# Performance work log

Measured on AMD Instinct MI355X. Metric: run time of the kernel, lower is better.

The kernel has to match this reference:

```python
import jax, jax.numpy as jnp
import numpy as np

HIDDEN = 32
N_STEPS = 64  # fixed-step RK4 replaces adaptive Dopri5 (same MLP-eval structure)
STD = 0.1     # init_params: Linear weights ~ N(0, 0.1), biases = 0


def _mlp(w1, b1, w2, b2, w3, b3, y):
    # NODE.forward: fc1 -> relu -> fc2 -> relu -> fc3 (t is unused in the source)
    h = jax.nn.relu(y @ w1 + b1)
    h = jax.nn.relu(h @ w2 + b2)
    return h @ w3 + b3


def setup_inputs() -> dict:
    key = jax.random.key(0)
    ks = jax.random.split(key, 8)
    B, D = 131072, 3
    x = jax.random.normal(ks[0], (B, D), dtype=jnp.float32)
    # eval times in (0.1, 1.0], sorted like a posterior-sample schedule
    samples = jnp.sort(
        jax.random.uniform(ks[1], (8, 1), jnp.float32, 0.1, 1.0), axis=0)
    w1 = (STD * jax.random.normal(ks[2], (D, HIDDEN))).astype(jnp.float32)
    b1 = jnp.zeros((HIDDEN,), jnp.float32)
    w2 = (STD * jax.random.normal(ks[3], (HIDDEN, HIDDEN))).astype(jnp.float32)
    b2 = jnp.zeros((HIDDEN,), jnp.float32)
    w3 = (STD * jax.random.normal(ks[4], (HIDDEN, D))).astype(jnp.float32)
    b3 = jnp.zeros((D,), jnp.float32)
    w_out = (STD * jax.random.normal(ks[5], (D, 1))).astype(jnp.float32)
    b_out = jnp.zeros((1,), jnp.float32)
    return {"x": x, "samples": samples, "w1": w1, "b1": b1, "w2": w2,
            "b2": b2, "w3": w3, "b3": b3, "w_out": w_out, "b_out": b_out}


def reference(x, samples, w1, b1, w2, b2, w3, b3, w_out, b_out):
    t_eval = samples[:, 0]                     # (S,)
    max_T = jnp.max(t_eval)
    dt = max_T / N_STEPS

    def step(y, _):
        k1 = _mlp(w1, b1, w2, b2, w3, b3, y)
        k2 = _mlp(w1, b1, w2, b2, w3, b3, y + 0.5 * dt * k1)
        k3 = _mlp(w1, b1, w2, b2, w3, b3, y + 0.5 * dt * k2)
        k4 = _mlp(w1, b1, w2, b2, w3, b3, y + dt * k3)
        y_new = y + (dt / 6.0) * (k1 + 2.0 * k2 + 2.0 * k3 + k4)
        return y_new, y_new

    # traj[i] is the state at time (i+1)*dt; shape (N_STEPS, B, 3)
    _, traj = jax.lax.scan(jax.checkpoint(step), x, jnp.arange(N_STEPS))

    # gather states at the grid step nearest each eval time
    idx = jnp.clip(jnp.round(t_eval / dt).astype(jnp.int32) - 1, 0, N_STEPS - 1)
    y_eval = traj[idx]                         # (S, B, 3)

    # fc_layers readout -> act_vec (S, B, 1)
    return y_eval @ w_out + b_out
```

## Files before the change

### kernel.cpp

```cpp
#include <hip/hip_runtime.h>

#define NSTEPS 64

typedef __attribute__((ext_vector_type(4)))  float  float4_;
typedef __attribute__((ext_vector_type(2)))  __fp16 half2_;
typedef __attribute__((ext_vector_type(8)))  __fp16 half8_;

__device__ __forceinline__ half2_ relu_pk_f16(float a, float b) {
    half2_ h = __builtin_amdgcn_cvt_pkrtz(a, b);
    return __builtin_elementwise_max(h, (half2_)(__fp16)0);
}

__global__ __launch_bounds__(256, 4)
void ode_rk4_mfma(const float* __restrict__ x,
                  const float* __restrict__ samples,
                  const float* __restrict__ w1, const float* __restrict__ b1,
                  const float* __restrict__ w2, const float* __restrict__ b2,
                  const float* __restrict__ w3, const float* __restrict__ b3,
                  const float* __restrict__ w_out, const float* __restrict__ b_out,
                  float* __restrict__ out, int B)
{
    const int lane  = threadIdx.x & 63;
    const int w     = threadIdx.x >> 6;
    const int col16 = lane & 15;
    const int quad  = lane >> 4;

    const int rowBase = (blockIdx.x * 4 + w) * 16;
    const int row = rowBase + col16;

    auto sig = [](int p) -> int {
        int q = (p & 15) >> 2, r = p & 3;
        return q * 8 + r + ((p < 16) ? 0 : 4);
    };

    const float maxT = samples[7];
    const float dt   = maxT / 64.0f;
    const float dt2  = 0.5f * dt;
    const float dt6  = dt / 6.0f;

    union F { half2_ h2[4]; half8_ h8; };

    F A1y[2];
#pragma unroll
    for (int H = 0; H < 2; ++H) {
        if (quad == 0) {
            int u = sig(16 * H + col16);
            A1y[H].h2[0] = (half2_){(__fp16)w1[0 * 32 + u], (__fp16)w1[1 * 32 + u]};
            A1y[H].h2[1] = (half2_){(__fp16)w1[2 * 32 + u], (__fp16)b1[u]};
            A1y[H].h2[2] = (half2_)(__fp16)0.0f;
            A1y[H].h2[3] = (half2_)(__fp16)0.0f;
        } else {
#pragma unroll
            for (int pp = 0; pp < 4; ++pp) A1y[H].h2[pp] = (half2_)(__fp16)0.0f;
        }
    }

    F Mh[2], Mf[2];
#pragma unroll
    for (int H = 0; H < 2; ++H) {
        int u = sig(16 * H + col16);
#pragma unroll
        for (int pp = 0; pp < 4; ++pp) {
            int kk = quad * 8 + 2 * pp;
            float m0 = w3[kk * 3 + 0] * w1[0 * 32 + u]
                     + w3[kk * 3 + 1] * w1[1 * 32 + u]
                     + w3[kk * 3 + 2] * w1[2 * 32 + u];
            float m1 = w3[(kk + 1) * 3 + 0] * w1[0 * 32 + u]
                     + w3[(kk + 1) * 3 + 1] * w1[1 * 32 + u]
                     + w3[(kk + 1) * 3 + 2] * w1[2 * 32 + u];
            Mh[H].h2[pp] = (half2_){(__fp16)(dt2 * m0), (__fp16)(dt2 * m1)};
            Mf[H].h2[pp] = (half2_){(__fp16)(dt  * m0), (__fp16)(dt  * m1)};
        }
    }

    F A2[2];
    float4_ Cb[2];
#pragma unroll
    for (int H = 0; H < 2; ++H) {
        int u = sig(16 * H + col16);
#pragma unroll
        for (int pp = 0; pp < 4; ++pp) {
            int kk = quad * 8 + 2 * pp;
            A2[H].h2[pp] = (half2_){(__fp16)w2[kk * 32 + u], (__fp16)w2[(kk + 1) * 32 + u]};
        }
#pragma unroll
        for (int r = 0; r < 4; ++r)
            Cb[H][r] = b2[sig(16 * H + quad * 4 + r)];
    }

    F A3;
    {
        const int  d    = col16 & 3;
        const bool live = d < 3;
#pragma unroll
        for (int pp = 0; pp < 4; ++pp) {
            int kk = quad * 8 + 2 * pp;
            A3.h2[pp] = live
                ? (half2_){(__fp16)w3[kk * 3 + d], (__fp16)w3[(kk + 1) * 3 + d]}
                : (half2_)(__fp16)0.0f;
        }
    }
    float4_ C3;
#pragma unroll
    for (int r = 0; r < 4; ++r)
        C3[r] = (r < 3) ? 6.0f * b3[r] : 0.0f;

    float4_ Zc;
#pragma unroll
    for (int r = 0; r < 4; ++r) Zc[r] = 0.0f;

    int sidx[8];
    unsigned long long smask = 0ull;
#pragma unroll
    for (int j = 0; j < 8; ++j) {
        int id = (int)rintf(samples[j] / dt) - 1;
        id = id < 0 ? 0 : (id > NSTEPS - 1 ? NSTEPS - 1 : id);
        id = __builtin_amdgcn_readfirstlane(id);
        sidx[j] = id;
        smask |= 1ull << id;
    }
    const float wo0 = w_out[0], wo1 = w_out[1], wo2 = w_out[2];
    const float bo  = b_out[0];
    const float cH0 = dt2 * b3[0], cH1 = dt2 * b3[1], cH2 = dt2 * b3[2];
    const float cF0 = dt  * b3[0], cF1 = dt  * b3[1], cF2 = dt  * b3[2];

    float y0 = x[(size_t)row * 3 + 0];
    float y1 = x[(size_t)row * 3 + 1];
    float y2 = x[(size_t)row * 3 + 2];

#pragma unroll 1
    for (int s = 0; s < NSTEPS; ++s) {
        half2_ b0a = __builtin_amdgcn_cvt_pkrtz(y0, y1);
        half2_ b0b = __builtin_amdgcn_cvt_pkrtz(y2, 1.0f);
        half2_ bHa = __builtin_amdgcn_cvt_pkrtz(y0 + cH0, y1 + cH1);
        half2_ bHb = __builtin_amdgcn_cvt_pkrtz(y2 + cH2, 1.0f);
        half2_ bFa = __builtin_amdgcn_cvt_pkrtz(y0 + cF0, y1 + cF1);
        half2_ bFb = __builtin_amdgcn_cvt_pkrtz(y2 + cF2, 1.0f);
        F By0, ByH, ByF;
        By0.h2[0] = b0a; By0.h2[1] = b0b; By0.h2[2] = b0a; By0.h2[3] = b0b;
        ByH.h2[0] = bHa; ByH.h2[1] = bHb; ByH.h2[2] = bHa; ByH.h2[3] = bHb;
        ByF.h2[0] = bFa; ByF.h2[1] = bFb; ByF.h2[2] = bFa; ByF.h2[3] = bFb;

        float4_ D1s0_0 = __builtin_amdgcn_mfma_f32_16x16x32_f16(A1y[0].h8, By0.h8, Zc, 0, 0, 0);
        float4_ D1s0_1 = __builtin_amdgcn_mfma_f32_16x16x32_f16(A1y[1].h8, By0.h8, Zc, 0, 0, 0);
        float4_ DbH0   = __builtin_amdgcn_mfma_f32_16x16x32_f16(A1y[0].h8, ByH.h8, Zc, 0, 0, 0);
        float4_ DbH1   = __builtin_amdgcn_mfma_f32_16x16x32_f16(A1y[1].h8, ByH.h8, Zc, 0, 0, 0);
        float4_ DbF0   = __builtin_amdgcn_mfma_f32_16x16x32_f16(A1y[0].h8, ByF.h8, Zc, 0, 0, 0);
        float4_ DbF1   = __builtin_amdgcn_mfma_f32_16x16x32_f16(A1y[1].h8, ByF.h8, Zc, 0, 0, 0);

        F Q, Sacc;

        {
            F P;
            P.h2[0] = relu_pk_f16(D1s0_0[0], D1s0_0[1]);
            P.h2[1] = relu_pk_f16(D1s0_0[2], D1s0_0[3]);
            P.h2[2] = relu_pk_f16(D1s0_1[0], D1s0_1[1]);
            P.h2[3] = relu_pk_f16(D1s0_1[2], D1s0_1[3]);
            float4_ D2_0 = __builtin_amdgcn_mfma_f32_16x16x32_f16(A2[0].h8, P.h8, Cb[0], 0, 0, 0);
            float4_ D2_1 = __builtin_amdgcn_mfma_f32_16x16x32_f16(A2[1].h8, P.h8, Cb[1], 0, 0, 0);
            Q.h2[0] = relu_pk_f16(D2_0[0], D2_0[1]);
            Q.h2[1] = relu_pk_f16(D2_0[2], D2_0[3]);
            Q.h2[2] = relu_pk_f16(D2_1[0], D2_1[1]);
            Q.h2[3] = relu_pk_f16(D2_1[2], D2_1[3]);
#pragma unroll
            for (int pp = 0; pp < 4; ++pp) Sacc.h2[pp] = Q.h2[pp];
        }

#pragma unroll
        for (int st = 1; st < 4; ++st) {
            float4_ D1_0, D1_1;
            if (st == 3) {
                D1_0 = __builtin_amdgcn_mfma_f32_16x16x32_f16(Mf[0].h8, Q.h8, DbF0, 0, 0, 0);
                D1_1 = __builtin_amdgcn_mfma_f32_16x16x32_f16(Mf[1].h8, Q.h8, DbF1, 0, 0, 0);
            } else {
                D1_0 = __builtin_amdgcn_mfma_f32_16x16x32_f16(Mh[0].h8, Q.h8, DbH0, 0, 0, 0);
                D1_1 = __builtin_amdgcn_mfma_f32_16x16x32_f16(Mh[1].h8, Q.h8, DbH1, 0, 0, 0);
            }
            F P;
            P.h2[0] = relu_pk_f16(D1_0[0], D1_0[1]);
            P.h2[1] = relu_pk_f16(D1_0[2], D1_0[3]);
            P.h2[2] = relu_pk_f16(D1_1[0], D1_1[1]);
            P.h2[3] = relu_pk_f16(D1_1[2], D1_1[3]);
            float4_ D2_0 = __builtin_amdgcn_mfma_f32_16x16x32_f16(A2[0].h8, P.h8, Cb[0], 0, 0, 0);
            float4_ D2_1 = __builtin_amdgcn_mfma_f32_16x16x32_f16(A2[1].h8, P.h8, Cb[1], 0, 0, 0);
            Q.h2[0] = relu_pk_f16(D2_0[0], D2_0[1]);
            Q.h2[1] = relu_pk_f16(D2_0[2], D2_0[3]);
            Q.h2[2] = relu_pk_f16(D2_1[0], D2_1[1]);
            Q.h2[3] = relu_pk_f16(D2_1[2], D2_1[3]);
            const __fp16 ca = (st == 3) ? (__fp16)1.0f : (__fp16)2.0f;
#pragma unroll
            for (int pp = 0; pp < 4; ++pp)
                Sacc.h2[pp] += ca * Q.h2[pp];
        }

        float4_ D3 = __builtin_amdgcn_mfma_f32_16x16x32_f16(A3.h8, Sacc.h8, C3, 0, 0, 0);
        y0 = fmaf(dt6, D3[0], y0);
        y1 = fmaf(dt6, D3[1], y1);
        y2 = fmaf(dt6, D3[2], y2);

        if ((smask >> s) & 1ull) {
            if (quad == 0) {
#pragma unroll
                for (int j = 0; j < 8; ++j) {
                    if (sidx[j] == s) {
                        out[(size_t)j * B + row] = fmaf(y2, wo2, fmaf(y1, wo1, fmaf(y0, wo0, bo)));
                    }
                }
            }
        }
    }
}

extern "C" void kernel_launch(void* const* d_in, const int* in_sizes, int n_in,
                              void* d_out, int out_size, void* d_ws, size_t ws_size,
                              hipStream_t stream) {
    const float* x       = (const float*)d_in[0];
    const float* samples = (const float*)d_in[1];
    const float* w1      = (const float*)d_in[2];
    const float* b1      = (const float*)d_in[3];
    const float* w2      = (const float*)d_in[4];
    const float* b2      = (const float*)d_in[5];
    const float* w3      = (const float*)d_in[6];
    const float* b3      = (const float*)d_in[7];
    const float* w_out   = (const float*)d_in[8];
    const float* b_out   = (const float*)d_in[9];
    float* out = (float*)d_out;

    const int B = in_sizes[0] / 3;
    const int rowsPerBlock = 64;
    const int grid = (B + rowsPerBlock - 1) / rowsPerBlock;
    ode_rk4_mfma<<<grid, 256, 0, stream>>>(
        x, samples, w1, b1, w2, b2, w3, b3, w_out, b_out, out, B);
}
```

Baseline: 211.3 us.

## Carry first-layer preactivation across RK4 steps, drop per-step layer-1 MFMAs

Keeps the first-layer preactivation z = W1·y + b1 as running state, updated each step by a fused MFMA (dt/6·W3W1 applied to the stage sum plus bias terms). This replaces the six per-step layer-1 MFMAs with two. The k4 stage reuses the half-step matrix with a doubled input instead of a separate full-step matrix. It also adds s_setprio around MFMA groups and switches to one-wave blocks of 16 rows. The carried z state drifts from the true W1·y in fp16/accumulated arithmetic, which risks accuracy over 64 steps.

```diff
diff --git a/kernel.cpp b/kernel.cpp
--- a/kernel.cpp
+++ b/kernel.cpp
@@ -11,7 +11,7 @@
     return __builtin_elementwise_max(h, (half2_)(__fp16)0);
 }
 
-__global__ __launch_bounds__(256, 4)
+__global__ __launch_bounds__(64, 4)
 void ode_rk4_mfma(const float* __restrict__ x,
                   const float* __restrict__ samples,
                   const float* __restrict__ w1, const float* __restrict__ b1,
@@ -21,12 +21,10 @@
                   float* __restrict__ out, int B)
 {
     const int lane  = threadIdx.x & 63;
-    const int w     = threadIdx.x >> 6;
     const int col16 = lane & 15;
     const int quad  = lane >> 4;
 
-    const int rowBase = (blockIdx.x * 4 + w) * 16;
-    const int row = rowBase + col16;
+    const int row = blockIdx.x * 16 + col16;
 
     auto sig = [](int p) -> int {
         int q = (p & 15) >> 2, r = p & 3;
@@ -40,22 +38,7 @@
 
     union F { half2_ h2[4]; half8_ h8; };
 
-    F A1y[2];
-#pragma unroll
-    for (int H = 0; H < 2; ++H) {
-        if (quad == 0) {
-            int u = sig(16 * H + col16);
-            A1y[H].h2[0] = (half2_){(__fp16)w1[0 * 32 + u], (__fp16)w1[1 * 32 + u]};
-            A1y[H].h2[1] = (half2_){(__fp16)w1[2 * 32 + u], (__fp16)b1[u]};
-            A1y[H].h2[2] = (half2_)(__fp16)0.0f;
-            A1y[H].h2[3] = (half2_)(__fp16)0.0f;
-        } else {
-#pragma unroll
-            for (int pp = 0; pp < 4; ++pp) A1y[H].h2[pp] = (half2_)(__fp16)0.0f;
-        }
-    }
-
-    F Mh[2], Mf[2];
+    F Mh[2], Mz[2];
 #pragma unroll
     for (int H = 0; H < 2; ++H) {
         int u = sig(16 * H + col16);
@@ -69,7 +52,7 @@
                      + w3[(kk + 1) * 3 + 1] * w1[1 * 32 + u]
                      + w3[(kk + 1) * 3 + 2] * w1[2 * 32 + u];
             Mh[H].h2[pp] = (half2_){(__fp16)(dt2 * m0), (__fp16)(dt2 * m1)};
-            Mf[H].h2[pp] = (half2_){(__fp16)(dt  * m0), (__fp16)(dt  * m1)};
+            Mz[H].h2[pp] = (half2_){(__fp16)(dt6 * m0), (__fp16)(dt6 * m1)};
         }
     }
 
@@ -105,9 +88,14 @@
     for (int r = 0; r < 4; ++r)
         C3[r] = (r < 3) ? 6.0f * b3[r] : 0.0f;
 
-    float4_ Zc;
-#pragma unroll
-    for (int r = 0; r < 4; ++r) Zc[r] = 0.0f;
+    float4_ cH[2];
+#pragma unroll
+    for (int H = 0; H < 2; ++H)
+#pragma unroll
+        for (int r = 0; r < 4; ++r) {
+            int u = sig(16 * H + quad * 4 + r);
+            cH[H][r] = dt2 * (b3[0] * w1[0 * 32 + u] + b3[1] * w1[1 * 32 + u] + b3[2] * w1[2 * 32 + u]);
+        }
 
     int sidx[8];
     unsigned long long smask = 0ull;
@@ -121,79 +109,119 @@
     }
     const float wo0 = w_out[0], wo1 = w_out[1], wo2 = w_out[2];
     const float bo  = b_out[0];
-    const float cH0 = dt2 * b3[0], cH1 = dt2 * b3[1], cH2 = dt2 * b3[2];
-    const float cF0 = dt  * b3[0], cF1 = dt  * b3[1], cF2 = dt  * b3[2];
 
     float y0 = x[(size_t)row * 3 + 0];
     float y1 = x[(size_t)row * 3 + 1];
     float y2 = x[(size_t)row * 3 + 2];
 
+    float4_ zb0, zb1;
+    {
+        F A1y[2];
+#pragma unroll
+        for (int H = 0; H < 2; ++H) {
+            if (quad == 0) {
+                int u = sig(16 * H + col16);
+                A1y[H].h2[0] = (half2_){(__fp16)w1[0 * 32 + u], (__fp16)w1[1 * 32 + u]};
+                A1y[H].h2[1] = (half2_){(__fp16)w1[2 * 32 + u], (__fp16)b1[u]};
+                A1y[H].h2[2] = (half2_)(__fp16)0.0f;
+                A1y[H].h2[3] = (half2_)(__fp16)0.0f;
+            } else {
+#pragma unroll
+                for (int pp = 0; pp < 4; ++pp) A1y[H].h2[pp] = (half2_)(__fp16)0.0f;
+            }
+        }
+        float4_ Zc;
+#pragma unroll
+        for (int r = 0; r < 4; ++r) Zc[r] = 0.0f;
+        half2_ b0a = __builtin_amdgcn_cvt_pkrtz(y0, y1);
+        half2_ b0b = __builtin_amdgcn_cvt_pkrtz(y2, 1.0f);
+        F By;
+        By.h2[0] = b0a; By.h2[1] = b0b; By.h2[2] = b0a; By.h2[3] = b0b;
+        zb0 = __builtin_amdgcn_mfma_f32_16x16x32_f16(A1y[0].h8, By.h8, Zc, 0, 0, 0);
+        zb1 = __builtin_amdgcn_mfma_f32_16x16x32_f16(A1y[1].h8, By.h8, Zc, 0, 0, 0);
+    }
+
+    const half2_ two = (half2_)(__fp16)2.0f;
+
 #pragma unroll 1
     for (int s = 0; s < NSTEPS; ++s) {
-        half2_ b0a = __builtin_amdgcn_cvt_pkrtz(y0, y1);
-        half2_ b0b = __builtin_amdgcn_cvt_pkrtz(y2, 1.0f);
-        half2_ bHa = __builtin_amdgcn_cvt_pkrtz(y0 + cH0, y1 + cH1);
-        half2_ bHb = __builtin_amdgcn_cvt_pkrtz(y2 + cH2, 1.0f);
-        half2_ bFa = __builtin_amdgcn_cvt_pkrtz(y0 + cF0, y1 + cF1);
-        half2_ bFb = __builtin_amdgcn_cvt_pkrtz(y2 + cF2, 1.0f);
-        F By0, ByH, ByF;
-        By0.h2[0] = b0a; By0.h2[1] = b0b; By0.h2[2] = b0a; By0.h2[3] = b0b;
-        ByH.h2[0] = bHa; ByH.h2[1] = bHb; ByH.h2[2] = bHa; ByH.h2[3] = bHb;
-        ByF.h2[0] = bFa; ByF.h2[1] = bFb; ByF.h2[2] = bFa; ByF.h2[3] = bFb;
-
-        float4_ D1s0_0 = __builtin_amdgcn_mfma_f32_16x16x32_f16(A1y[0].h8, By0.h8, Zc, 0, 0, 0);
-        float4_ D1s0_1 = __builtin_amdgcn_mfma_f32_16x16x32_f16(A1y[1].h8, By0.h8, Zc, 0, 0, 0);
-        float4_ DbH0   = __builtin_amdgcn_mfma_f32_16x16x32_f16(A1y[0].h8, ByH.h8, Zc, 0, 0, 0);
-        float4_ DbH1   = __builtin_amdgcn_mfma_f32_16x16x32_f16(A1y[1].h8, ByH.h8, Zc, 0, 0, 0);
-        float4_ DbF0   = __builtin_amdgcn_mfma_f32_16x16x32_f16(A1y[0].h8, ByF.h8, Zc, 0, 0, 0);
-        float4_ DbF1   = __builtin_amdgcn_mfma_f32_16x16x32_f16(A1y[1].h8, ByF.h8, Zc, 0, 0, 0);
-
-        F Q, Sacc;
-
-        {
-            F P;
-            P.h2[0] = relu_pk_f16(D1s0_0[0], D1s0_0[1]);
-            P.h2[1] = relu_pk_f16(D1s0_0[2], D1s0_0[3]);
-            P.h2[2] = relu_pk_f16(D1s0_1[0], D1s0_1[1]);
-            P.h2[3] = relu_pk_f16(D1s0_1[2], D1s0_1[3]);
-            float4_ D2_0 = __builtin_amdgcn_mfma_f32_16x16x32_f16(A2[0].h8, P.h8, Cb[0], 0, 0, 0);
-            float4_ D2_1 = __builtin_amdgcn_mfma_f32_16x16x32_f16(A2[1].h8, P.h8, Cb[1], 0, 0, 0);
-            Q.h2[0] = relu_pk_f16(D2_0[0], D2_0[1]);
-            Q.h2[1] = relu_pk_f16(D2_0[2], D2_0[3]);
-            Q.h2[2] = relu_pk_f16(D2_1[0], D2_1[1]);
-            Q.h2[3] = relu_pk_f16(D2_1[2], D2_1[3]);
-#pragma unroll
-            for (int pp = 0; pp < 4; ++pp) Sacc.h2[pp] = Q.h2[pp];
-        }
-
-#pragma unroll
-        for (int st = 1; st < 4; ++st) {
-            float4_ D1_0, D1_1;
-            if (st == 3) {
-                D1_0 = __builtin_amdgcn_mfma_f32_16x16x32_f16(Mf[0].h8, Q.h8, DbF0, 0, 0, 0);
-                D1_1 = __builtin_amdgcn_mfma_f32_16x16x32_f16(Mf[1].h8, Q.h8, DbF1, 0, 0, 0);
-            } else {
-                D1_0 = __builtin_amdgcn_mfma_f32_16x16x32_f16(Mh[0].h8, Q.h8, DbH0, 0, 0, 0);
-                D1_1 = __builtin_amdgcn_mfma_f32_16x16x32_f16(Mh[1].h8, Q.h8, DbH1, 0, 0, 0);
-            }
-            F P;
+        F P, Q, S;
+
+        P.h2[0] = relu_pk_f16(zb0[0], zb0[1]);
+        P.h2[1] = relu_pk_f16(zb0[2], zb0[3]);
+        P.h2[2] = relu_pk_f16(zb1[0], zb1[1]);
+        P.h2[3] = relu_pk_f16(zb1[2], zb1[3]);
+        __builtin_amdgcn_s_setprio(1);
+        float4_ D2_0 = __builtin_amdgcn_mfma_f32_16x16x32_f16(A2[0].h8, P.h8, Cb[0], 0, 0, 0);
+        float4_ D2_1 = __builtin_amdgcn_mfma_f32_16x16x32_f16(A2[1].h8, P.h8, Cb[1], 0, 0, 0);
+        __builtin_amdgcn_s_setprio(0);
+        Q.h2[0] = relu_pk_f16(D2_0[0], D2_0[1]);
+        Q.h2[1] = relu_pk_f16(D2_0[2], D2_0[3]);
+        Q.h2[2] = relu_pk_f16(D2_1[0], D2_1[1]);
+        Q.h2[3] = relu_pk_f16(D2_1[2], D2_1[3]);
+#pragma unroll
+        for (int pp = 0; pp < 4; ++pp) S.h2[pp] = Q.h2[pp];
+
+        float4_ zh0 = zb0 + cH[0];
+        float4_ zh1 = zb1 + cH[1];
+
+#pragma unroll
+        for (int st = 1; st <= 2; ++st) {
+            __builtin_amdgcn_s_setprio(1);
+            float4_ D1_0 = __builtin_amdgcn_mfma_f32_16x16x32_f16(Mh[0].h8, Q.h8, zh0, 0, 0, 0);
+            float4_ D1_1 = __builtin_amdgcn_mfma_f32_16x16x32_f16(Mh[1].h8, Q.h8, zh1, 0, 0, 0);
+            __builtin_amdgcn_s_setprio(0);
             P.h2[0] = relu_pk_f16(D1_0[0], D1_0[1]);
             P.h2[1] = relu_pk_f16(D1_0[2], D1_0[3]);
             P.h2[2] = relu_pk_f16(D1_1[0], D1_1[1]);
             P.h2[3] = relu_pk_f16(D1_1[2], D1_1[3]);
-            float4_ D2_0 = __builtin_amdgcn_mfma_f32_16x16x32_f16(A2[0].h8, P.h8, Cb[0], 0, 0, 0);
-            float4_ D2_1 = __builtin_amdgcn_mfma_f32_16x16x32_f16(A2[1].h8, P.h8, Cb[1], 0, 0, 0);
-            Q.h2[0] = relu_pk_f16(D2_0[0], D2_0[1]);
-            Q.h2[1] = relu_pk_f16(D2_0[2], D2_0[3]);
-            Q.h2[2] = relu_pk_f16(D2_1[0], D2_1[1]);
-            Q.h2[3] = relu_pk_f16(D2_1[2], D2_1[3]);
-            const __fp16 ca = (st == 3) ? (__fp16)1.0f : (__fp16)2.0f;
+            __builtin_amdgcn_s_setprio(1);
+            float4_ E0 = __builtin_amdgcn_mfma_f32_16x16x32_f16(A2[0].h8, P.h8, Cb[0], 0, 0, 0);
+            float4_ E1 = __builtin_amdgcn_mfma_f32_16x16x32_f16(A2[1].h8, P.h8, Cb[1], 0, 0, 0);
+            __builtin_amdgcn_s_setprio(0);
+            Q.h2[0] = relu_pk_f16(E0[0], E0[1]);
+            Q.h2[1] = relu_pk_f16(E0[2], E0[3]);
+            Q.h2[2] = relu_pk_f16(E1[0], E1[1]);
+            Q.h2[3] = relu_pk_f16(E1[2], E1[3]);
 #pragma unroll
             for (int pp = 0; pp < 4; ++pp)
-                Sacc.h2[pp] += ca * Q.h2[pp];
-        }
-
-        float4_ D3 = __builtin_amdgcn_mfma_f32_16x16x32_f16(A3.h8, Sacc.h8, C3, 0, 0, 0);
+                S.h2[pp] += two * Q.h2[pp];
+        }
+
+        zh0 = zh0 + cH[0];
+        zh1 = zh1 + cH[1];
+        F Qd;
+#pragma unroll
+        for (int pp = 0; pp < 4; ++pp) Qd.h2[pp] = Q.h2[pp] + Q.h2[pp];
+        __builtin_amdgcn_s_setprio(1);
+        float4_ D1_0 = __builtin_amdgcn_mfma_f32_16x16x32_f16(Mh[0].h8, Qd.h8, zh0, 0, 0, 0);
+        float4_ D1_1 = __builtin_amdgcn_mfma_f32_16x16x32_f16(Mh[1].h8, Qd.h8, zh1, 0, 0, 0);
+        __builtin_amdgcn_s_setprio(0);
+        P.h2[0] = relu_pk_f16(D1_0[0], D1_0[1]);
+        P.h2[1] = relu_pk_f16(D1_0[2], D1_0[3]);
+        P.h2[2] = relu_pk_f16(D1_1[0], D1_1[1]);
+        P.h2[3] = relu_pk_f16(D1_1[2], D1_1[3]);
+        __builtin_amdgcn_s_setprio(1);
+        float4_ E0 = __builtin_amdgcn_mfma_f32_16x16x32_f16(A2[0].h8, P.h8, Cb[0], 0, 0, 0);
+        float4_ E1 = __builtin_amdgcn_mfma_f32_16x16x32_f16(A2[1].h8, P.h8, Cb[1], 0, 0, 0);
+        __builtin_amdgcn_s_setprio(0);
+        Q.h2[0] = relu_pk_f16(E0[0], E0[1]);
+        Q.h2[1] = relu_pk_f16(E0[2], E0[3]);
+        Q.h2[2] = relu_pk_f16(E1[0], E1[1]);
+        Q.h2[3] = relu_pk_f16(E1[2], E1[3]);
+#pragma unroll
+        for (int pp = 0; pp < 4; ++pp) S.h2[pp] += Q.h2[pp];
+
+        __builtin_amdgcn_s_setprio(1);
+        float4_ D3 = __builtin_amdgcn_mfma_f32_16x16x32_f16(A3.h8, S.h8, C3, 0, 0, 0);
+        zb0 = __builtin_amdgcn_mfma_f32_16x16x32_f16(Mz[0].h8, S.h8, zb0, 0, 0, 0);
+        zb1 = __builtin_amdgcn_mfma_f32_16x16x32_f16(Mz[1].h8, S.h8, zb1, 0, 0, 0);
+        __builtin_amdgcn_s_setprio(0);
+#pragma unroll
+        for (int r = 0; r < 4; ++r) {
+            zb0[r] = fmaf(2.0f, cH[0][r], zb0[r]);
+            zb1[r] = fmaf(2.0f, cH[1][r], zb1[r]);
+        }
         y0 = fmaf(dt6, D3[0], y0);
         y1 = fmaf(dt6, D3[1], y1);
         y2 = fmaf(dt6, D3[2], y2);
@@ -227,8 +255,8 @@
     float* out = (float*)d_out;
 
     const int B = in_sizes[0] / 3;
-    const int rowsPerBlock = 64;
+    const int rowsPerBlock = 16;
     const int grid = (B + rowsPerBlock - 1) / rowsPerBlock;
-    ode_rk4_mfma<<<grid, 256, 0, stream>>>(
+    ode_rk4_mfma<<<grid, 64, 0, stream>>>(
         x, samples, w1, b1, w2, b2, w3, b3, w_out, b_out, out, B);
 }
```

Result: no change. 208.9 us (-1.2%).
